# Performance work log

Measured on AMD Instinct MI355X. Metric: run time of the kernel, lower is better.

Reference implementation:

```python
import jax, jax.numpy as jnp
import numpy as np

# ---- configuration (mirrors cfg used by the torch module) ----
H = W = 64          # cfg.KEYPOINT.HEATMAP_SIZE
C = 256             # cfg.KEYPOINT.NFEATS
N = 2               # batch (number of view pairs)
S = 32              # cfg.EPIPOLAR.SAMPLESIZE
DS = 4              # cfg.BACKBONE.DOWNSAMPLE
EPS = 1e-3          # self.epsilon


def pix2coord(v):
    # feature-map pixel -> original-image coordinate
    return v * DS + DS / 2.0 - 0.5


def _camera_pair():
    # realistic stereo pair: image is 256x256 (64x64 heatmap * downsample 4)
    K = np.array([[300.0, 0.0, 127.5], [0.0, 300.0, 127.5], [0.0, 0.0, 1.0]])
    P1 = K @ np.hstack([np.eye(3), np.zeros((3, 1))])
    ang = np.deg2rad(15.0)
    R = np.array([[np.cos(ang), 0, np.sin(ang)], [0, 1, 0], [-np.sin(ang), 0, np.cos(ang)]])
    t = np.array([[-0.5], [0.0], [0.1]])
    P2 = K @ np.hstack([R, t])
    return P1.astype(np.float32), P2.astype(np.float32)


def setup_inputs() -> dict:
    key = jax.random.key(0)
    k1, k2 = jax.random.split(key)
    feat1 = jax.random.normal(k1, (N, C, H, W), dtype=jnp.float32)
    feat2 = jax.random.normal(k2, (N, C, H, W), dtype=jnp.float32)
    P1np, P2np = _camera_pair()
    P1 = jnp.asarray(np.stack([P1np] * N))
    P2 = jnp.asarray(np.stack([P2np] * N))
    return {"feat1": feat1, "feat2": feat2, "P1": P1, "P2": P2}


def _fundamental(P1, P2):
    # F = [e2]_x P2 P1^+ ; camera center = null vector of P1
    P1inv = jnp.linalg.pinv(P1)          # 4x3
    _, _, Vt = jnp.linalg.svd(P1)
    Cc = Vt[-1]                          # homogeneous camera center, (4,)
    e2 = P2 @ Cc                         # epipole in view 2, (3,)
    z = jnp.zeros(())
    skew = jnp.stack([jnp.stack([z, -e2[2], e2[1]]),
                      jnp.stack([e2[2], z, -e2[0]]),
                      jnp.stack([-e2[1], e2[0], z])])
    return skew @ (P2 @ P1inv)


def _sample_locs(P1, P2):
    """Epipolar-line sample locations, [S, N, H, W, 2] normalized to [-1,1]."""
    xs = pix2coord(jnp.arange(W, dtype=jnp.float32))
    ys = pix2coord(jnp.arange(H, dtype=jnp.float32))
    xmin, xmax = xs[0], xs[-1]
    ymin, ymax = ys[0], ys[-1]
    gy, gx = jnp.meshgrid(ys, xs, indexing='ij')
    grid = jnp.stack([gx.ravel(), gy.ravel(), jnp.ones(H * W, jnp.float32)])

    F = jax.vmap(_fundamental)(P1, P2)
    lines = jnp.einsum('nij,jp->nip', F, grid)
    a, b, c = lines[:, 0], lines[:, 1], lines[:, 2]
    a_s = jnp.where(jnp.abs(a) < EPS, EPS, a)
    b_s = jnp.where(jnp.abs(b) < EPS, EPS, b)
    # intersections of a*x + b*y + c = 0 with the 4 image borders
    y_at_xmin = -(c + a * xmin) / b_s
    y_at_xmax = -(c + a * xmax) / b_s
    x_at_ymin = -(c + b * ymin) / a_s
    x_at_ymax = -(c + b * ymax) / a_s
    cx = jnp.stack([jnp.full_like(a, xmin), jnp.full_like(a, xmax), x_at_ymin, x_at_ymax], -1)  # N,HW,4
    cy = jnp.stack([y_at_xmin, y_at_xmax, jnp.full_like(a, ymin), jnp.full_like(a, ymax)], -1)
    tol = 1e-2
    valid = (cx >= xmin - tol) & (cx <= xmax + tol) & (cy >= ymin - tol) & (cy <= ymax + tol)
    # invalid -> far out of range (equivalent of self.outrange_tensor);
    # such sample locs fall outside [-1,1] and contribute zeros in grid_sample
    cx = jnp.where(valid, cx, xmin - 10000.0)
    cy = jnp.where(valid, cy, ymin - 10000.0)
    order = jnp.argsort(jnp.logical_not(valid), axis=-1)  # stable: valid candidates first
    pick = order[..., :2]                                 # N,HW,2
    px = jnp.take_along_axis(cx, pick, axis=-1)
    py = jnp.take_along_axis(cy, pick, axis=-1)
    # normalize original-image coords to [-1,1] over the feature grid extent
    nx = (px - xmin) / (xmax - xmin) * 2.0 - 1.0
    ny = (py - ymin) / (ymax - ymin) * 2.0 - 1.0
    start = jnp.stack([nx[..., 0], ny[..., 0]], -1)       # N,HW,2
    end = jnp.stack([nx[..., 1], ny[..., 1]], -1)
    steps = jnp.linspace(0.0, 1.0, S).reshape(S, 1, 1, 1)
    locs = start[None] + steps * (end - start)[None]      # S,N,HW,2
    return locs.reshape(S, N, H, W, 2)


def _grid_sample(img, grid):
    """Bilinear sampling with zeros padding. img [C,H,W], grid [S,H,W,2] -> [S,C,H,W]."""
    gx, gy = grid[..., 0], grid[..., 1]
    x = (gx + 1.0) * 0.5 * (W - 1)
    y = (gy + 1.0) * 0.5 * (H - 1)
    x0 = jnp.floor(x)
    y0 = jnp.floor(y)
    wx = x - x0
    wy = y - y0
    x0i = x0.astype(jnp.int32)
    y0i = y0.astype(jnp.int32)

    def gather(yi, xi, w):
        inb = (yi >= 0) & (yi <= H - 1) & (xi >= 0) & (xi <= W - 1)
        yc = jnp.clip(yi, 0, H - 1)
        xc = jnp.clip(xi, 0, W - 1)
        vals = img[:, yc, xc]                  # C,S,H,W
        return vals * (w * inb)[None]

    out = (gather(y0i, x0i, (1 - wy) * (1 - wx))
           + gather(y0i, x0i + 1, (1 - wy) * wx)
           + gather(y0i + 1, x0i, wy * (1 - wx))
           + gather(y0i + 1, x0i + 1, wy * wx))
    return out.transpose(1, 0, 2, 3)           # S,C,H,W


def reference(feat1, feat2, P1, P2):
    # geometry (torch.no_grad in original)
    locs = jax.lax.stop_gradient(_sample_locs(P1, P2))   # S,N,H,W,2
    locs_n = jnp.transpose(locs, (1, 0, 2, 3, 4))        # N,S,H,W,2
    sampled = jax.vmap(_grid_sample)(feat2, locs_n)      # N,S,C,H,W
    # dot-product similarity + softmax attention over the epipolar samples ('avg')
    sim = jax.nn.softmax(jnp.einsum('nchw,nschw->nshw', feat1, sampled), axis=1)
    out = jnp.einsum('nshw,nschw->nchw', sim, sampled)   # N,C,H,W
    return out
```

## Files before the change

kernel.cpp:

```cpp
#include <hip/hip_runtime.h>
#include <math.h>

#define H 64
#define W 64
#define C 256
#define NB 2
#define SS 32
#define HW (H*W)

typedef __attribute__((ext_vector_type(8))) _Float16 half8;
typedef __attribute__((ext_vector_type(2))) _Float16 half2v;

__device__ void fmat_compute(const float* __restrict__ P1f,
                             const float* __restrict__ P2f,
                             double* __restrict__ Fout, int n) {
  double p1[3][4], p2[3][4];
  for (int i = 0; i < 3; ++i)
    for (int j = 0; j < 4; ++j) {
      p1[i][j] = (double)P1f[n * 12 + i * 4 + j];
      p2[i][j] = (double)P2f[n * 12 + i * 4 + j];
    }
  double A[3][3];
  for (int i = 0; i < 3; ++i)
    for (int j = 0; j < 3; ++j) {
      double s = 0;
      for (int k = 0; k < 4; ++k) s += p1[i][k] * p1[j][k];
      A[i][j] = s;
    }
  double det = A[0][0] * (A[1][1] * A[2][2] - A[1][2] * A[2][1])
             - A[0][1] * (A[1][0] * A[2][2] - A[1][2] * A[2][0])
             + A[0][2] * (A[1][0] * A[2][1] - A[1][1] * A[2][0]);
  double id = 1.0 / det;
  double Ai[3][3];
  Ai[0][0] = (A[1][1] * A[2][2] - A[1][2] * A[2][1]) * id;
  Ai[0][1] = (A[0][2] * A[2][1] - A[0][1] * A[2][2]) * id;
  Ai[0][2] = (A[0][1] * A[1][2] - A[0][2] * A[1][1]) * id;
  Ai[1][0] = (A[1][2] * A[2][0] - A[1][0] * A[2][2]) * id;
  Ai[1][1] = (A[0][0] * A[2][2] - A[0][2] * A[2][0]) * id;
  Ai[1][2] = (A[0][2] * A[1][0] - A[0][0] * A[1][2]) * id;
  Ai[2][0] = (A[1][0] * A[2][1] - A[1][1] * A[2][0]) * id;
  Ai[2][1] = (A[0][1] * A[2][0] - A[0][0] * A[2][1]) * id;
  Ai[2][2] = (A[0][0] * A[1][1] - A[0][1] * A[1][0]) * id;
  double Pi[4][3];
  for (int i = 0; i < 4; ++i)
    for (int j = 0; j < 3; ++j) {
      double s = 0;
      for (int k = 0; k < 3; ++k) s += p1[k][i] * Ai[k][j];
      Pi[i][j] = s;
    }
  double M[3][3];
  for (int i = 0; i < 3; ++i)
    for (int j = 0; j < 3; ++j) {
      double s = 0;
      for (int k = 0; k < 4; ++k) s += p2[i][k] * Pi[k][j];
      M[i][j] = s;
    }
  double nv[4];
  {
    auto det3 = [&](int ca, int cb, int cc) {
      return p1[0][ca] * (p1[1][cb] * p1[2][cc] - p1[1][cc] * p1[2][cb])
           - p1[0][cb] * (p1[1][ca] * p1[2][cc] - p1[1][cc] * p1[2][ca])
           + p1[0][cc] * (p1[1][ca] * p1[2][cb] - p1[1][cb] * p1[2][ca]);
    };
    nv[0] =  det3(1, 2, 3);
    nv[1] = -det3(0, 2, 3);
    nv[2] =  det3(0, 1, 3);
    nv[3] = -det3(0, 1, 2);
  }
  double nn = sqrt(nv[0]*nv[0] + nv[1]*nv[1] + nv[2]*nv[2] + nv[3]*nv[3]);
  for (int i = 0; i < 4; ++i) nv[i] /= nn;
  double e2[3];
  for (int i = 0; i < 3; ++i) {
    double s = 0;
    for (int j = 0; j < 4; ++j) s += p2[i][j] * nv[j];
    e2[i] = s;
  }
  for (int j = 0; j < 3; ++j) {
    Fout[n * 9 + 0 * 3 + j] = -e2[2] * M[1][j] + e2[1] * M[2][j];
    Fout[n * 9 + 1 * 3 + j] =  e2[2] * M[0][j] - e2[0] * M[2][j];
    Fout[n * 9 + 2 * 3 + j] = -e2[1] * M[0][j] + e2[0] * M[1][j];
  }
}

__global__ __launch_bounds__(256) void prep_kernel(
    const float* __restrict__ feat2,
    const float* __restrict__ P1f, const float* __restrict__ P2f,
    _Float16* __restrict__ f2t, double* __restrict__ Fd) {
  __shared__ float tile[32][33];
  const int n  = blockIdx.z;
  const int p0 = blockIdx.x * 32;
  const int c0 = blockIdx.y * 32;
  const int tx = threadIdx.x, ty = threadIdx.y;
  const float* src = feat2 + (size_t)n * (C * HW);
#pragma unroll
  for (int j = 0; j < 4; ++j) {
    int cc = c0 + ty + j * 8;
    tile[ty + j * 8][tx] = src[(size_t)cc * HW + p0 + tx];
  }
  __syncthreads();
  {
    const int tid = ty * 32 + tx;
    const int pp = tid >> 3;
    const int cp = tid & 7;
    _Float16* dst = f2t + (size_t)n * (HW * C) + (size_t)(p0 + pp) * C + c0;
#pragma unroll
    for (int jj = 0; jj < 2; ++jj) {
      const int cc = (cp + jj * 8) * 2;
      half2v h2;
      h2.x = (_Float16)tile[cc][pp];
      h2.y = (_Float16)tile[cc + 1][pp];
      *(half2v*)(dst + cc) = h2;
    }
  }
  if (n == 0 && blockIdx.x == 0 && blockIdx.y == 0) {
    int t = ty * 32 + tx;
    if (t < NB) fmat_compute(P1f, P2f, Fd, t);
  }
}

struct Stage {
  half8 a0, a1, b0, b1, c0, c1, d0, d1;
  float w00, w01, w10, w11;
};

__global__ __launch_bounds__(256) void epi_main(
    const float* __restrict__ feat1, const _Float16* __restrict__ f2t,
    const double* __restrict__ Fd, float* __restrict__ out) {
  const int tid  = threadIdx.x;
  const int lane = tid & 63;
  const int qtr  = tid >> 6;
  const int grp  = lane >> 4;
  const int cl   = lane & 15;
  const int bid  = blockIdx.x;
  const int r    = bid & 7;
  const int k    = bid >> 3;
  const int n    = r >> 2;
  const int sub  = r & 3;
  const int p    = (sub * 256 + k) * 4 + grp;
  const int h = p >> 6, w = p & (W - 1);

  float f1r[16];
  {
    const float* f1b = feat1 + ((size_t)n * C + cl * 8) * HW + p;
#pragma unroll
    for (int i = 0; i < 8; ++i) {
      f1r[i]     = f1b[(size_t)i * HW];
      f1r[8 + i] = f1b[(size_t)(128 + i) * HW];
    }
  }

  const double* Fdp = Fd + n * 9;
  const float F0 = (float)Fdp[0], F1 = (float)Fdp[1], F2 = (float)Fdp[2];
  const float F3 = (float)Fdp[3], F4 = (float)Fdp[4], F5 = (float)Fdp[5];
  const float F6 = (float)Fdp[6], F7 = (float)Fdp[7], F8 = (float)Fdp[8];
  const float X = w * 4.0f + 1.5f;
  const float Y = h * 4.0f + 1.5f;
  const float a = F0 * X + F1 * Y + F2;
  const float b = F3 * X + F4 * Y + F5;
  const float c = F6 * X + F7 * Y + F8;
  const float a_s = (fabsf(a) < 1e-3f) ? 1e-3f : a;
  const float b_s = (fabsf(b) < 1e-3f) ? 1e-3f : b;
  const float xmin = 1.5f, xmax = 253.5f, ymin = 1.5f, ymax = 253.5f, tol = 0.01f;
  float cx[4], cy[4];
  cx[0] = xmin;  cy[0] = -(c + a * xmin) / b_s;
  cx[1] = xmax;  cy[1] = -(c + a * xmax) / b_s;
  cx[2] = -(c + b * ymin) / a_s;  cy[2] = ymin;
  cx[3] = -(c + b * ymax) / a_s;  cy[3] = ymax;
  bool valid[4];
#pragma unroll
  for (int i = 0; i < 4; ++i)
    valid[i] = (cx[i] >= xmin - tol) && (cx[i] <= xmax + tol) &&
               (cy[i] >= ymin - tol) && (cy[i] <= ymax + tol);
#pragma unroll
  for (int i = 0; i < 4; ++i)
    if (!valid[i]) { cx[i] = xmin - 10000.0f; cy[i] = ymin - 10000.0f; }
  int pk0 = -1, pk1 = -1;
#pragma unroll
  for (int i = 0; i < 4; ++i)
    if (valid[i]) { if (pk0 < 0) pk0 = i; else if (pk1 < 0) pk1 = i; }
#pragma unroll
  for (int i = 0; i < 4; ++i)
    if (!valid[i]) { if (pk0 < 0) pk0 = i; else if (pk1 < 0) pk1 = i; }
  const float x0p = (cx[pk0] - 1.5f) * 0.25f;
  const float y0p = (cy[pk0] - 1.5f) * 0.25f;
  const float pdx = (cx[pk1] - 1.5f) * 0.25f - x0p;
  const float pdy = (cy[pk1] - 1.5f) * 0.25f - y0p;

  const _Float16* f2b = f2t + (size_t)n * HW * C + cl * 8;

  float m = -1e30f, l = 0.f;
  float acc[16];
#pragma unroll
  for (int i = 0; i < 16; ++i) acc[i] = 0.f;

  auto issue = [&](int s, Stage& st) {
    const float t = (float)s * (1.0f / 31.0f);
    const float x = fmaf(t, pdx, x0p);
    const float y = fmaf(t, pdy, y0p);
    const float xf = floorf(x), yf = floorf(y);
    const float wx = x - xf, wy = y - yf;
    const int x0 = (int)xf, y0 = (int)yf;
    const bool bx0 = ((unsigned)x0 < W), bx1 = ((unsigned)(x0 + 1) < W);
    const bool by0 = ((unsigned)y0 < H), by1 = ((unsigned)(y0 + 1) < H);
    const int xc0 = min(max(x0, 0), W - 1);
    const int yc0 = min(max(y0, 0), H - 1);
    const float u0 = 1.f - wx, v0 = 1.f - wy;
    st.w00 = v0 * u0 * (float)(bx0 & by0);
    st.w01 = v0 * wx * (float)(bx1 & by0);
    st.w10 = wy * u0 * (float)(bx0 & by1);
    st.w11 = wy * wx * (float)(bx1 & by1);
    const _Float16* q00 = f2b + (yc0 * W + xc0) * C;
    const _Float16* q10 = q00 + W * C;
    st.a0 = *(const half8*)(q00);
    st.a1 = *(const half8*)(q00 + 128);
    st.b0 = *(const half8*)(q00 + 256);
    st.b1 = *(const half8*)(q00 + 384);
    st.c0 = *(const half8*)(q10);
    st.c1 = *(const half8*)(q10 + 128);
    st.d0 = *(const half8*)(q10 + 256);
    st.d1 = *(const half8*)(q10 + 384);
  };

  auto process = [&](const Stage& st) {
    float q[16];
#pragma unroll
    for (int i = 0; i < 8; ++i) {
      q[i] = fmaf((float)st.a0[i], st.w00, fmaf((float)st.b0[i], st.w01,
             fmaf((float)st.c0[i], st.w10, (float)st.d0[i] * st.w11)));
      q[8 + i] = fmaf((float)st.a1[i], st.w00, fmaf((float)st.b1[i], st.w01,
                 fmaf((float)st.c1[i], st.w10, (float)st.d1[i] * st.w11)));
    }
    float part = 0.f;
#pragma unroll
    for (int i = 0; i < 16; ++i) part = fmaf(f1r[i], q[i], part);
    part += __shfl_xor(part, 1);
    part += __shfl_xor(part, 2);
    part += __shfl_xor(part, 4);
    part += __shfl_xor(part, 8);

    if (__any(part > m + 8.f)) {
      const float mn = fmaxf(m, part);
      const float sc = __expf(m - mn);
      l *= sc;
#pragma unroll
      for (int i = 0; i < 16; ++i) acc[i] *= sc;
      m = mn;
    }
    const float e = __expf(part - m);
    l += e;
#pragma unroll
    for (int i = 0; i < 16; ++i) acc[i] = fmaf(e, q[i], acc[i]);
  };

  Stage sA, sB;
  const int s0 = qtr * (SS / 4);
  issue(s0, sA);
#pragma unroll
  for (int j = 0; j < SS / 4; ++j) {
    if (j < SS / 4 - 1) issue(s0 + j + 1, ((j + 1) & 1) ? sB : sA);
    process((j & 1) ? sB : sA);
  }

  __shared__ float lsm[3][64][18];
  if (qtr) {
#pragma unroll
    for (int i = 0; i < 16; ++i) lsm[qtr - 1][lane][i] = acc[i];
    lsm[qtr - 1][lane][16] = m;
    lsm[qtr - 1][lane][17] = l;
  }
  __syncthreads();
  if (!qtr) {
    float mf = m;
#pragma unroll
    for (int kk = 0; kk < 3; ++kk) mf = fmaxf(mf, lsm[kk][lane][16]);
    const float s0e = __expf(m - mf);
    float L = l * s0e;
    float o[16];
#pragma unroll
    for (int i = 0; i < 16; ++i) o[i] = acc[i] * s0e;
#pragma unroll
    for (int kk = 0; kk < 3; ++kk) {
      const float sk = __expf(lsm[kk][lane][16] - mf);
      L = fmaf(lsm[kk][lane][17], sk, L);
#pragma unroll
      for (int i = 0; i < 16; ++i) o[i] = fmaf(lsm[kk][lane][i], sk, o[i]);
    }
    const float inv = 1.0f / L;
    float* ob = out + (size_t)n * C * HW + p + (size_t)(cl * 8) * HW;
#pragma unroll
    for (int i = 0; i < 8; ++i) {
      ob[(size_t)i * HW]         = o[i] * inv;
      ob[(size_t)(128 + i) * HW] = o[8 + i] * inv;
    }
  }
}

extern "C" void kernel_launch(void* const* d_in, const int* in_sizes, int n_in,
                              void* d_out, int out_size, void* d_ws, size_t ws_size,
                              hipStream_t stream) {
  const float* feat1 = (const float*)d_in[0];
  const float* feat2 = (const float*)d_in[1];
  const float* P1 = (const float*)d_in[2];
  const float* P2 = (const float*)d_in[3];
  float* out = (float*)d_out;

  char* ws = (char*)d_ws;
  _Float16* f2t = (_Float16*)ws;
  double*   Fd  = (double*)(ws + (5u << 20));

  prep_kernel<<<dim3(HW / 32, C / 32, NB), dim3(32, 8), 0, stream>>>(
      feat2, P1, P2, f2t, Fd);
  epi_main<<<NB * HW / 4, 256, 0, stream>>>(feat1, f2t, Fd, out);
}
```

Before: 47.84 us.

## Remap epilogue work to 32 lanes per pixel with fp16 bilinear math

Each wave now handles two pixels, using 32 lanes of 8 channels each, and walks all 32 epipolar samples itself. This removes the cross-wave online-softmax merge through shared memory and the __syncthreads. Bilinear interpolation is done in packed half precision with half-precision weights, and the per-pixel dot reduction uses DPP/swizzle instead of shfl. Loads are triple-buffered, and the grid is halved. The tradeoffs are a longer serial dependency chain per wave and reduced precision in the interpolation.

Result: faster. 43.28 us (-9.5%).

```diff
diff --git a/kernel.cpp b/kernel.cpp
--- a/kernel.cpp
+++ b/kernel.cpp
@@ -118,9 +118,23 @@
   }
 }
 
+__device__ __forceinline__ float groupsum32(float v) {
+  v += __int_as_float(__builtin_amdgcn_update_dpp(
+         0, __float_as_int(v), 0xB1, 0xF, 0xF, true));
+  v += __int_as_float(__builtin_amdgcn_update_dpp(
+         0, __float_as_int(v), 0x4E, 0xF, 0xF, true));
+  v += __int_as_float(__builtin_amdgcn_update_dpp(
+         0, __float_as_int(v), 0x124, 0xF, 0xF, true));
+  v += __int_as_float(__builtin_amdgcn_update_dpp(
+         0, __float_as_int(v), 0x128, 0xF, 0xF, true));
+  v += __int_as_float(__builtin_amdgcn_ds_swizzle(
+         __float_as_int(v), 0x401F));
+  return v;
+}
+
 struct Stage {
-  half8 a0, a1, b0, b1, c0, c1, d0, d1;
-  float w00, w01, w10, w11;
+  half8 a, b, c, d;
+  _Float16 w00, w01, w10, w11;
 };
 
 __global__ __launch_bounds__(256) void epi_main(
@@ -128,25 +142,23 @@
     const double* __restrict__ Fd, float* __restrict__ out) {
   const int tid  = threadIdx.x;
   const int lane = tid & 63;
-  const int qtr  = tid >> 6;
-  const int grp  = lane >> 4;
-  const int cl   = lane & 15;
+  const int wv   = tid >> 6;
+  const int grp  = lane >> 5;
+  const int cl   = lane & 31;
   const int bid  = blockIdx.x;
   const int r    = bid & 7;
   const int k    = bid >> 3;
   const int n    = r >> 2;
   const int sub  = r & 3;
-  const int p    = (sub * 256 + k) * 4 + grp;
+  const int p    = (sub * 128 + k) * 8 + wv * 2 + grp;
   const int h = p >> 6, w = p & (W - 1);
-
-  float f1r[16];
+  const int cb = cl * 8;
+
+  float f1r[8];
   {
-    const float* f1b = feat1 + ((size_t)n * C + cl * 8) * HW + p;
-#pragma unroll
-    for (int i = 0; i < 8; ++i) {
-      f1r[i]     = f1b[(size_t)i * HW];
-      f1r[8 + i] = f1b[(size_t)(128 + i) * HW];
-    }
+    const float* f1b = feat1 + ((size_t)n * C + cb) * HW + p;
+#pragma unroll
+    for (int i = 0; i < 8; ++i) f1r[i] = f1b[(size_t)i * HW];
   }
 
   const double* Fdp = Fd + n * 9;
@@ -186,12 +198,12 @@
   const float pdx = (cx[pk1] - 1.5f) * 0.25f - x0p;
   const float pdy = (cy[pk1] - 1.5f) * 0.25f - y0p;
 
-  const _Float16* f2b = f2t + (size_t)n * HW * C + cl * 8;
+  const _Float16* f2b = f2t + (size_t)n * HW * C + cb;
 
   float m = -1e30f, l = 0.f;
-  float acc[16];
-#pragma unroll
-  for (int i = 0; i < 16; ++i) acc[i] = 0.f;
+  float acc[8];
+#pragma unroll
+  for (int i = 0; i < 8; ++i) acc[i] = 0.f;
 
   auto issue = [&](int s, Stage& st) {
     const float t = (float)s * (1.0f / 31.0f);
@@ -203,96 +215,60 @@
     const bool bx0 = ((unsigned)x0 < W), bx1 = ((unsigned)(x0 + 1) < W);
     const bool by0 = ((unsigned)y0 < H), by1 = ((unsigned)(y0 + 1) < H);
     const int xc0 = min(max(x0, 0), W - 1);
+    const int xc1 = min(max(x0 + 1, 0), W - 1);
     const int yc0 = min(max(y0, 0), H - 1);
+    const int yc1 = min(max(y0 + 1, 0), H - 1);
     const float u0 = 1.f - wx, v0 = 1.f - wy;
-    st.w00 = v0 * u0 * (float)(bx0 & by0);
-    st.w01 = v0 * wx * (float)(bx1 & by0);
-    st.w10 = wy * u0 * (float)(bx0 & by1);
-    st.w11 = wy * wx * (float)(bx1 & by1);
-    const _Float16* q00 = f2b + (yc0 * W + xc0) * C;
-    const _Float16* q10 = q00 + W * C;
-    st.a0 = *(const half8*)(q00);
-    st.a1 = *(const half8*)(q00 + 128);
-    st.b0 = *(const half8*)(q00 + 256);
-    st.b1 = *(const half8*)(q00 + 384);
-    st.c0 = *(const half8*)(q10);
-    st.c1 = *(const half8*)(q10 + 128);
-    st.d0 = *(const half8*)(q10 + 256);
-    st.d1 = *(const half8*)(q10 + 384);
+    st.w00 = (_Float16)(v0 * u0 * (float)(bx0 & by0));
+    st.w01 = (_Float16)(v0 * wx * (float)(bx1 & by0));
+    st.w10 = (_Float16)(wy * u0 * (float)(bx0 & by1));
+    st.w11 = (_Float16)(wy * wx * (float)(bx1 & by1));
+    const int r0 = yc0 * W, r1 = yc1 * W;
+    st.a = *(const half8*)(f2b + (r0 + xc0) * C);
+    st.b = *(const half8*)(f2b + (r0 + xc1) * C);
+    st.c = *(const half8*)(f2b + (r1 + xc0) * C);
+    st.d = *(const half8*)(f2b + (r1 + xc1) * C);
   };
 
   auto process = [&](const Stage& st) {
-    float q[16];
-#pragma unroll
-    for (int i = 0; i < 8; ++i) {
-      q[i] = fmaf((float)st.a0[i], st.w00, fmaf((float)st.b0[i], st.w01,
-             fmaf((float)st.c0[i], st.w10, (float)st.d0[i] * st.w11)));
-      q[8 + i] = fmaf((float)st.a1[i], st.w00, fmaf((float)st.b1[i], st.w01,
-                 fmaf((float)st.c1[i], st.w10, (float)st.d1[i] * st.w11)));
-    }
+    half8 qh = st.a * st.w00 + st.b * st.w01 + st.c * st.w10 + st.d * st.w11;
     float part = 0.f;
 #pragma unroll
-    for (int i = 0; i < 16; ++i) part = fmaf(f1r[i], q[i], part);
-    part += __shfl_xor(part, 1);
-    part += __shfl_xor(part, 2);
-    part += __shfl_xor(part, 4);
-    part += __shfl_xor(part, 8);
+    for (int i = 0; i < 8; ++i) part = fmaf(f1r[i], (float)qh[i], part);
+    part = groupsum32(part);
 
     if (__any(part > m + 8.f)) {
       const float mn = fmaxf(m, part);
       const float sc = __expf(m - mn);
       l *= sc;
 #pragma unroll
-      for (int i = 0; i < 16; ++i) acc[i] *= sc;
+      for (int i = 0; i < 8; ++i) acc[i] *= sc;
       m = mn;
     }
     const float e = __expf(part - m);
     l += e;
 #pragma unroll
-    for (int i = 0; i < 16; ++i) acc[i] = fmaf(e, q[i], acc[i]);
+    for (int i = 0; i < 8; ++i) acc[i] = fmaf(e, (float)qh[i], acc[i]);
   };
 
-  Stage sA, sB;
-  const int s0 = qtr * (SS / 4);
-  issue(s0, sA);
-#pragma unroll
-  for (int j = 0; j < SS / 4; ++j) {
-    if (j < SS / 4 - 1) issue(s0 + j + 1, ((j + 1) & 1) ? sB : sA);
-    process((j & 1) ? sB : sA);
-  }
-
-  __shared__ float lsm[3][64][18];
-  if (qtr) {
-#pragma unroll
-    for (int i = 0; i < 16; ++i) lsm[qtr - 1][lane][i] = acc[i];
-    lsm[qtr - 1][lane][16] = m;
-    lsm[qtr - 1][lane][17] = l;
-  }
-  __syncthreads();
-  if (!qtr) {
-    float mf = m;
-#pragma unroll
-    for (int kk = 0; kk < 3; ++kk) mf = fmaxf(mf, lsm[kk][lane][16]);
-    const float s0e = __expf(m - mf);
-    float L = l * s0e;
-    float o[16];
-#pragma unroll
-    for (int i = 0; i < 16; ++i) o[i] = acc[i] * s0e;
-#pragma unroll
-    for (int kk = 0; kk < 3; ++kk) {
-      const float sk = __expf(lsm[kk][lane][16] - mf);
-      L = fmaf(lsm[kk][lane][17], sk, L);
-#pragma unroll
-      for (int i = 0; i < 16; ++i) o[i] = fmaf(lsm[kk][lane][i], sk, o[i]);
-    }
-    const float inv = 1.0f / L;
-    float* ob = out + (size_t)n * C * HW + p + (size_t)(cl * 8) * HW;
-#pragma unroll
-    for (int i = 0; i < 8; ++i) {
-      ob[(size_t)i * HW]         = o[i] * inv;
-      ob[(size_t)(128 + i) * HW] = o[8 + i] * inv;
-    }
-  }
+  Stage sA, sB, sC;
+  issue(0, sA);
+  issue(1, sB);
+  for (int k3 = 0; k3 < 30; k3 += 3) {
+    issue(k3 + 2, sC);
+    process(sA);
+    issue(k3 + 3, sA);
+    process(sB);
+    issue(k3 + 4, sB);
+    process(sC);
+  }
+  process(sA);
+  process(sB);
+
+  const float inv = 1.0f / l;
+  float* ob = out + (size_t)n * C * HW + (size_t)cb * HW + p;
+#pragma unroll
+  for (int i = 0; i < 8; ++i) ob[(size_t)i * HW] = acc[i] * inv;
 }
 
 extern "C" void kernel_launch(void* const* d_in, const int* in_sizes, int n_in,
@@ -310,5 +286,5 @@
 
   prep_kernel<<<dim3(HW / 32, C / 32, NB), dim3(32, 8), 0, stream>>>(
       feat2, P1, P2, f2t, Fd);
-  epi_main<<<NB * HW / 4, 256, 0, stream>>>(feat1, f2t, Fd, out);
-}
+  epi_main<<<NB * HW / 8, 256, 0, stream>>>(feat1, f2t, Fd, out);
+}
```
